# Performance work log

Measured on AMD Instinct MI355X. Metric: run time of the kernel, lower is better.

The kernel has to match this reference:

```python
import jax, jax.numpy as jnp
import numpy as np

S, B, C, HD = 3, 64, 256, 256
ZS, XS = 7, 31
EPS = 1e-5


def _bn(x, g, b, m, v):
    # inference-mode BatchNorm2d on NCHW
    inv = g / jnp.sqrt(v + EPS)
    return x * inv[None, :, None, None] + (b - m * inv)[None, :, None, None]


def _dw3(x, w):
    # depthwise 3x3 conv, VALID padding, groups = channels; w: [C,1,3,3]
    return jax.lax.conv_general_dilated(
        x, w, (1, 1), 'VALID', feature_group_count=x.shape[1],
        dimension_numbers=('NCHW', 'OIHW', 'NCHW'))


def _xcorr_depthwise(x, k):
    # Siamese depthwise cross-correlation: groups = batch*channels
    b, c, h, w = x.shape
    o = jax.lax.conv_general_dilated(
        x.reshape(1, b * c, h, w),
        k.reshape(b * c, 1, k.shape[2], k.shape[3]),
        (1, 1), 'VALID', feature_group_count=b * c,
        dimension_numbers=('NCHW', 'OIHW', 'NCHW'))
    return o.reshape(b, c, o.shape[2], o.shape[3])


def _c1(x, w):
    # 1x1 conv, no bias; w: [O,C]
    return jnp.einsum('bchw,oc->bohw', x, w)


def _forward(z_fs, x_fs, pre_w, pre_g, pre_b, pre_m, pre_v,
             head_w, head_g, head_b, head_m, head_v,
             cls_w1, cls_g, cls_b, cls_m, cls_v, cls_w2, cls_b2,
             loc_w1, loc_g, loc_b, loc_m, loc_v, loc_w2, loc_b2,
             ctr_w1, ctr_g, ctr_b, ctr_m, ctr_v, ctr_w2, ctr_b2,
             w_cls, w_loc, w_ctr):
    relu = jax.nn.relu
    cls_l, loc_l, ctr_l = [], [], []
    for i in range(S):
        search = relu(_bn(_dw3(x_fs[i], pre_w[i]), pre_g[i], pre_b[i], pre_m[i], pre_v[i]))
        kernel = relu(_bn(_dw3(z_fs[i], pre_w[i]), pre_g[i], pre_b[i], pre_m[i], pre_v[i]))
        feat = relu(_bn(_c1(_xcorr_depthwise(search, kernel), head_w[i]),
                        head_g[i], head_b[i], head_m[i], head_v[i]))

        def hd(w1, g, b, m, v, w2, b2):
            h = relu(_bn(_c1(feat, w1), g, b, m, v))
            return _c1(h, w2) + b2[None, :, None, None]

        cls_l.append(hd(cls_w1[i], cls_g[i], cls_b[i], cls_m[i], cls_v[i], cls_w2[i], cls_b2[i]))
        loc_l.append(hd(loc_w1[i], loc_g[i], loc_b[i], loc_m[i], loc_v[i], loc_w2[i], loc_b2[i]))
        ctr_l.append(hd(ctr_w1[i], ctr_g[i], ctr_b[i], ctr_m[i], ctr_v[i], ctr_w2[i], ctr_b2[i]))

    wc = jax.nn.softmax(w_cls)
    wl = jax.nn.softmax(w_loc)
    wt = jax.nn.softmax(w_ctr)
    cls = sum(cls_l[i] * wc[i] for i in range(S))
    loc = sum(loc_l[i] * wl[i] for i in range(S))
    ctr = sum(ctr_l[i] * wt[i] for i in range(S))
    return cls, loc, ctr


def setup_inputs() -> dict:
    key = jax.random.key(0)
    ks = iter(jax.random.split(key, 64))

    def rn(shape, scale=0.05):
        return jax.random.normal(next(ks), shape, jnp.float32) * scale

    def bn_params(n):
        return (jnp.ones((S, n), jnp.float32), jnp.zeros((S, n), jnp.float32),
                rn((S, n), 0.1), jax.random.uniform(next(ks), (S, n), jnp.float32) + 0.5)

    inp = {}
    inp['z_fs'] = rn((S, B, C, ZS, ZS), 1.0)
    inp['x_fs'] = rn((S, B, C, XS, XS), 1.0)
    inp['pre_w'] = rn((S, C, 1, 3, 3), 0.2)
    inp['pre_g'], inp['pre_b'], inp['pre_m'], inp['pre_v'] = bn_params(C)
    inp['head_w'] = rn((S, HD, C))
    inp['head_g'], inp['head_b'], inp['head_m'], inp['head_v'] = bn_params(HD)
    for nm, co in (('cls', 2), ('loc', 4), ('ctr', 1)):
        inp[nm + '_w1'] = rn((S, HD, HD))
        inp[nm + '_g'], inp[nm + '_b'], inp[nm + '_m'], inp[nm + '_v'] = bn_params(HD)
        inp[nm + '_w2'] = rn((S, co, HD))
        inp[nm + '_b2'] = jnp.zeros((S, co), jnp.float32)
    inp['w_cls'] = jnp.ones((S,), jnp.float32)
    inp['w_loc'] = jnp.ones((S,), jnp.float32)
    inp['w_ctr'] = jnp.ones((S,), jnp.float32)
    return inp


def reference(z_fs, x_fs, pre_w, pre_g, pre_b, pre_m, pre_v,
              head_w, head_g, head_b, head_m, head_v,
              cls_w1, cls_g, cls_b, cls_m, cls_v, cls_w2, cls_b2,
              loc_w1, loc_g, loc_b, loc_m, loc_v, loc_w2, loc_b2,
              ctr_w1, ctr_g, ctr_b, ctr_m, ctr_v, ctr_w2, ctr_b2,
              w_cls, w_loc, w_ctr):
    return _forward(z_fs, x_fs, pre_w, pre_g, pre_b, pre_m, pre_v,
                    head_w, head_g, head_b, head_m, head_v,
                    cls_w1, cls_g, cls_b, cls_m, cls_v, cls_w2, cls_b2,
                    loc_w1, loc_g, loc_b, loc_m, loc_v, loc_w2, loc_b2,
                    ctr_w1, ctr_g, ctr_b, ctr_m, ctr_v, ctr_w2, ctr_b2,
                    w_cls, w_loc, w_ctr)
```

## Files before the change

### kernel.cpp

```cpp
#include <hip/hip_runtime.h>
#include <hip/hip_bf16.h>

using bf16 = __hip_bfloat16;

#define B_  64
#define C_  256
#define HD_ 256
#define XS  31
#define XO  29
#define ZS  7
#define ZO  5
#define OSP 25
#define XO2 (XO*XO)
#define ZO2 (ZO*ZO)
#define OS2 (OSP*OSP)
#define EPSF 1e-5f

typedef __attribute__((ext_vector_type(4))) float f32x4;
typedef __attribute__((ext_vector_type(8))) short s16x8;

__device__ __forceinline__ unsigned short f2bf(float f) {
    union { float f; unsigned int u; } a; a.f = f;
    unsigned int r = a.u + 0x7FFF + ((a.u >> 16) & 1);
    return (unsigned short)(r >> 16);
}
__device__ __forceinline__ unsigned int pk2(unsigned short a, unsigned short b) {
    return (unsigned int)a | ((unsigned int)b << 16);
}

__global__ void wconv_k(const float* __restrict__ hw, const float* __restrict__ cw,
                        const float* __restrict__ lw, const float* __restrict__ tw,
                        unsigned short* __restrict__ o)
{
    int i = blockIdx.x * 256 + threadIdx.x;
    if (i >= 4 * 196608) return;
    int seg = i / 196608, r = i - seg * 196608;
    const float* s = (seg == 0) ? hw : (seg == 1) ? cw : (seg == 2) ? lw : tw;
    o[i] = f2bf(s[r]);
}

__global__ __launch_bounds__(256) void fused_pre_xcorr(
    const float* __restrict__ x, const float* __restrict__ z,
    const float* __restrict__ w, const float* __restrict__ g,
    const float* __restrict__ bb, const float* __restrict__ mm,
    const float* __restrict__ vv, unsigned short* __restrict__ out,
    int si_base)
{
    const int zs  = blockIdx.y;
    const int si  = si_base + zs;
    const int bc  = blockIdx.x;
    const int c   = bc & (C_ - 1);
    const int tid = threadIdx.x;

    __shared__ float xt[31 * 33 + 16];
    __shared__ float st[29 * 36 + 8];
    __shared__ float zt[49];
    __shared__ float ktl[25];
    __shared__ float wtl[9];

    const float* xp = x + ((size_t)si * B_ * C_ + bc) * (XS * XS);
    for (int j = tid; j < XS * XS; j += 256) xt[(j / 31) * 33 + (j % 31)] = xp[j];
    if (tid < 49) zt[tid] = z[((size_t)si * B_ * C_ + bc) * 49 + tid];
    if (tid < 9)  wtl[tid] = w[((size_t)si * C_ + c) * 9 + tid];
    const int cg = si * C_ + c;
    const float inv  = g[cg] * rsqrtf(vv[cg] + EPSF);
    const float beta = bb[cg] - mm[cg] * inv;
    __syncthreads();

    float wr[9];
    #pragma unroll
    for (int j = 0; j < 9; ++j) wr[j] = wtl[j];

    if (tid < 25) {
        int oy = tid / 5, ox = tid - (tid / 5) * 5;
        float a = 0.f;
        #pragma unroll
        for (int dy = 0; dy < 3; ++dy)
            #pragma unroll
            for (int dx = 0; dx < 3; ++dx)
                a += zt[(oy + dy) * ZS + ox + dx] * wr[dy * 3 + dx];
        ktl[tid] = fmaxf(a * inv + beta, 0.f);
    }

    if (tid < 232) {
        int r = tid >> 3, c0 = (tid & 7) * 4;
        float o0 = 0.f, o1 = 0.f, o2 = 0.f, o3 = 0.f;
        #pragma unroll
        for (int dy = 0; dy < 3; ++dy) {
            const float* row = &xt[(r + dy) * 33 + c0];
            float v0 = row[0], v1 = row[1], v2 = row[2],
                  v3 = row[3], v4 = row[4], v5 = row[5];
            float w0 = wr[dy * 3], w1 = wr[dy * 3 + 1], w2 = wr[dy * 3 + 2];
            o0 += v0 * w0 + v1 * w1 + v2 * w2;
            o1 += v1 * w0 + v2 * w1 + v3 * w2;
            o2 += v2 * w0 + v3 * w1 + v4 * w2;
            o3 += v3 * w0 + v4 * w1 + v5 * w2;
        }
        float4 res;
        res.x = fmaxf(o0 * inv + beta, 0.f);
        res.y = fmaxf(o1 * inv + beta, 0.f);
        res.z = fmaxf(o2 * inv + beta, 0.f);
        res.w = fmaxf(o3 * inv + beta, 0.f);
        *(float4*)&st[r * 36 + c0] = res;
    }
    __syncthreads();

    if (tid < 125) {
        float kt[25];
        #pragma unroll
        for (int j = 0; j < 25; ++j) kt[j] = ktl[j];
        int u = tid / 5, v0 = (tid - (tid / 5) * 5) * 5;
        float o0 = 0.f, o1 = 0.f, o2 = 0.f, o3 = 0.f, o4 = 0.f;
        #pragma unroll
        for (int p = 0; p < 5; ++p) {
            const float* row = &st[(u + p) * 36 + v0];
            float r0 = row[0], r1 = row[1], r2 = row[2], r3 = row[3], r4 = row[4],
                  r5 = row[5], r6 = row[6], r7 = row[7], r8 = row[8];
            float k0 = kt[p * 5], k1 = kt[p * 5 + 1], k2 = kt[p * 5 + 2],
                  k3 = kt[p * 5 + 3], k4 = kt[p * 5 + 4];
            o0 += r0 * k0 + r1 * k1 + r2 * k2 + r3 * k3 + r4 * k4;
            o1 += r1 * k0 + r2 * k1 + r3 * k2 + r4 * k3 + r5 * k4;
            o2 += r2 * k0 + r3 * k1 + r4 * k2 + r5 * k3 + r6 * k4;
            o3 += r3 * k0 + r4 * k1 + r5 * k2 + r6 * k3 + r7 * k4;
            o4 += r4 * k0 + r5 * k1 + r6 * k2 + r7 * k3 + r8 * k4;
        }
        unsigned short* op = out + ((size_t)zs * B_ * C_ + bc) * OS2 + u * OSP + v0;
        op[0] = f2bf(o0); op[1] = f2bf(o1); op[2] = f2bf(o2);
        op[3] = f2bf(o3); op[4] = f2bf(o4);
    }
}

__global__ __launch_bounds__(256) void c1_mfma(
    const unsigned short* __restrict__ X,
    const float* __restrict__ W,
    const unsigned short* __restrict__ Wbf,
    const float* __restrict__ g, const float* __restrict__ bb,
    const float* __restrict__ mm, const float* __restrict__ vv,
    unsigned short* __restrict__ out, int si_base)
{
    __shared__ unsigned short Abuf[4 * 128 * 8];
    __shared__ unsigned short Bbuf[4 * 128 * 8];
    __shared__ float s_inv[128], s_beta[128];

    const int tid  = threadIdx.x;
    const int wave = tid >> 6, lane = tid & 63;
    const int quad = lane >> 4, l16 = lane & 15;
    const int sb = blockIdx.x * 128;
    const int ob = blockIdx.y * 128;
    const int zs = blockIdx.z >> 6;
    const int si = si_base + zs;
    const int b  = blockIdx.z & 63;
    const int wm = (wave & 1) * 64, wn = (wave >> 1) * 64;

    const float* gs  = g  + (size_t)si * HD_;
    const float* bbs = bb + (size_t)si * HD_;
    const float* mms = mm + (size_t)si * HD_;
    const float* vvs = vv + (size_t)si * HD_;
    const float* Ws  = W  + (size_t)si * HD_ * C_;
    const unsigned short* Wbs = Wbf ? Wbf + (size_t)si * HD_ * C_ : nullptr;

    if (tid < 128) {
        int o = ob + tid;
        float iv = gs[o] * rsqrtf(vvs[o] + EPSF);
        s_inv[tid]  = iv;
        s_beta[tid] = bbs[o] - mms[o] * iv;
    }

    const int sm = tid & 127;
    const int kh = tid >> 7;
    const unsigned short* Xb = X + ((size_t)zs * B_ + b) * C_ * OS2;
    const bool npred = (sb + sm) < OS2;

    f32x4 acc[4][4];
    #pragma unroll
    for (int i = 0; i < 4; ++i)
        #pragma unroll
        for (int j = 0; j < 4; ++j)
            acc[i][j] = (f32x4){0.f, 0.f, 0.f, 0.f};

    for (int kk = 0; kk < C_; kk += 32) {
        uint4 pa0, pa1;
        if (Wbs) {
            const unsigned short* wp = Wbs + (size_t)(ob + sm) * C_ + kk + kh * 16;
            pa0 = *(const uint4*)(wp);
            pa1 = *(const uint4*)(wp + 8);
        } else {
            const float* wp = Ws + (size_t)(ob + sm) * C_ + kk + kh * 16;
            float4 w0 = *(const float4*)(wp + 0);
            float4 w1 = *(const float4*)(wp + 4);
            float4 w2 = *(const float4*)(wp + 8);
            float4 w3 = *(const float4*)(wp + 12);
            pa0.x = pk2(f2bf(w0.x), f2bf(w0.y)); pa0.y = pk2(f2bf(w0.z), f2bf(w0.w));
            pa0.z = pk2(f2bf(w1.x), f2bf(w1.y)); pa0.w = pk2(f2bf(w1.z), f2bf(w1.w));
            pa1.x = pk2(f2bf(w2.x), f2bf(w2.y)); pa1.y = pk2(f2bf(w2.z), f2bf(w2.w));
            pa1.z = pk2(f2bf(w3.x), f2bf(w3.y)); pa1.w = pk2(f2bf(w3.z), f2bf(w3.w));
        }
        *(uint4*)&Abuf[((kh * 2 + 0) * 128 + sm) * 8] = pa0;
        *(uint4*)&Abuf[((kh * 2 + 1) * 128 + sm) * 8] = pa1;

        unsigned short bu[16];
        #pragma unroll
        for (int j = 0; j < 16; ++j)
            bu[j] = npred ? Xb[(size_t)(kk + kh * 16 + j) * OS2 + sb + sm]
                          : (unsigned short)0;
        uint4 pb0, pb1;
        pb0.x = pk2(bu[0],  bu[1]);  pb0.y = pk2(bu[2],  bu[3]);
        pb0.z = pk2(bu[4],  bu[5]);  pb0.w = pk2(bu[6],  bu[7]);
        pb1.x = pk2(bu[8],  bu[9]);  pb1.y = pk2(bu[10], bu[11]);
        pb1.z = pk2(bu[12], bu[13]); pb1.w = pk2(bu[14], bu[15]);
        *(uint4*)&Bbuf[((kh * 2 + 0) * 128 + sm) * 8] = pb0;
        *(uint4*)&Bbuf[((kh * 2 + 1) * 128 + sm) * 8] = pb1;

        __syncthreads();

        s16x8 af[4], bfr[4];
        #pragma unroll
        for (int mt = 0; mt < 4; ++mt)
            af[mt] = *(const s16x8*)&Abuf[(quad * 128 + wm + mt * 16 + l16) * 8];
        #pragma unroll
        for (int nt = 0; nt < 4; ++nt)
            bfr[nt] = *(const s16x8*)&Bbuf[(quad * 128 + wn + nt * 16 + l16) * 8];
        #pragma unroll
        for (int mt = 0; mt < 4; ++mt)
            #pragma unroll
            for (int nt = 0; nt < 4; ++nt)
                acc[mt][nt] = __builtin_amdgcn_mfma_f32_16x16x32_bf16(
                    af[mt], bfr[nt], acc[mt][nt], 0, 0, 0);

        __syncthreads();
    }

    #pragma unroll
    for (int mt = 0; mt < 4; ++mt) {
        #pragma unroll
        for (int r = 0; r < 4; ++r) {
            int orow = wm + mt * 16 + quad * 4 + r;
            float iv = s_inv[orow], be = s_beta[orow];
            size_t obase = (((size_t)zs * B_ + b) * HD_ + (ob + orow)) * OS2;
            #pragma unroll
            for (int nt = 0; nt < 4; ++nt) {
                int s = sb + wn + nt * 16 + l16;
                if (s < OS2)
                    out[obase + s] = f2bf(fmaxf(acc[mt][nt][r] * iv + be, 0.f));
            }
        }
    }
}

__global__ __launch_bounds__(256) void heads3_mfma(
    const unsigned short* __restrict__ feat,
    const float* __restrict__ w1c, const float* __restrict__ w1l, const float* __restrict__ w1t,
    const unsigned short* __restrict__ Wbf,
    const float* __restrict__ gc, const float* __restrict__ bc2, const float* __restrict__ mc, const float* __restrict__ vc,
    const float* __restrict__ gl, const float* __restrict__ bl, const float* __restrict__ ml, const float* __restrict__ vl,
    const float* __restrict__ gt, const float* __restrict__ bt, const float* __restrict__ mt2, const float* __restrict__ vt,
    const float* __restrict__ w2c, const float* __restrict__ w2l, const float* __restrict__ w2t,
    const float* __restrict__ wvc, const float* __restrict__ wvl, const float* __restrict__ wvt,
    int si_base, float* __restrict__ oacc)
{
    __shared__ unsigned short Abuf[4 * 128 * 8];
    __shared__ unsigned short Bbuf[4 * 128 * 8];
    __shared__ float s_inv[128], s_beta[128];
    __shared__ float s_w2[4 * 256];

    const int tid  = threadIdx.x;
    const int wave = tid >> 6, lane = tid & 63;
    const int quad = lane >> 4, l16 = lane & 15;
    const int sb   = blockIdx.x * 128;
    const int by   = blockIdx.y;
    const int head = by >> 1;
    const int lob  = (by & 1) * 128;
    const int zs   = blockIdx.z >> 6;
    const int si   = si_base + zs;
    const int b    = blockIdx.z & 63;
    const int wm = (wave & 1) * 64, wn = (wave >> 1) * 64;

    const float* W  = (head == 0) ? w1c : (head == 1) ? w1l : w1t;
    const float* g  = (head == 0) ? gc  : (head == 1) ? gl  : gt;
    const float* bb = (head == 0) ? bc2 : (head == 1) ? bl  : bt;
    const float* mm = (head == 0) ? mc  : (head == 1) ? ml  : mt2;
    const float* vv = (head == 0) ? vc  : (head == 1) ? vl  : vt;
    const float* w2 = (head == 0) ? w2c : (head == 1) ? w2l : w2t;
    const float* wv = (head == 0) ? wvc : (head == 1) ? wvl : wvt;
    const int  CON  = (head == 0) ? 2 : (head == 1) ? 4 : 1;

    const float* Ws  = W + (size_t)si * HD_ * C_;
    const unsigned short* Wbs =
        Wbf ? Wbf + (size_t)(head + 1) * (3 * HD_ * C_) + (size_t)si * HD_ * C_ : nullptr;
    g  += (size_t)si * HD_;  bb += (size_t)si * HD_;
    mm += (size_t)si * HD_;  vv += (size_t)si * HD_;
    w2 += (size_t)si * CON * HD_;

    if (tid < 128) {
        int o = lob + tid;
        float iv = g[o] * rsqrtf(vv[o] + EPSF);
        s_inv[tid]  = iv;
        s_beta[tid] = bb[o] - mm[o] * iv;
    }
    for (int t = tid; t < CON * 256; t += 256) s_w2[t] = w2[t];

    const int sm = tid & 127;
    const int kh = tid >> 7;
    const unsigned short* Xb = feat + ((size_t)zs * B_ + b) * C_ * OS2;
    const bool npred = (sb + sm) < OS2;

    f32x4 acc[4][4];
    #pragma unroll
    for (int i = 0; i < 4; ++i)
        #pragma unroll
        for (int j = 0; j < 4; ++j)
            acc[i][j] = (f32x4){0.f, 0.f, 0.f, 0.f};

    for (int kk = 0; kk < C_; kk += 32) {
        uint4 pa0, pa1;
        if (Wbs) {
            const unsigned short* wp = Wbs + (size_t)(lob + sm) * C_ + kk + kh * 16;
            pa0 = *(const uint4*)(wp);
            pa1 = *(const uint4*)(wp + 8);
        } else {
            const float* wp = Ws + (size_t)(lob + sm) * C_ + kk + kh * 16;
            float4 w0 = *(const float4*)(wp + 0);
            float4 w1 = *(const float4*)(wp + 4);
            float4 w2v4 = *(const float4*)(wp + 8);
            float4 w3 = *(const float4*)(wp + 12);
            pa0.x = pk2(f2bf(w0.x), f2bf(w0.y)); pa0.y = pk2(f2bf(w0.z), f2bf(w0.w));
            pa0.z = pk2(f2bf(w1.x), f2bf(w1.y)); pa0.w = pk2(f2bf(w1.z), f2bf(w1.w));
            pa1.x = pk2(f2bf(w2v4.x), f2bf(w2v4.y)); pa1.y = pk2(f2bf(w2v4.z), f2bf(w2v4.w));
            pa1.z = pk2(f2bf(w3.x), f2bf(w3.y)); pa1.w = pk2(f2bf(w3.z), f2bf(w3.w));
        }
        *(uint4*)&Abuf[((kh * 2 + 0) * 128 + sm) * 8] = pa0;
        *(uint4*)&Abuf[((kh * 2 + 1) * 128 + sm) * 8] = pa1;

        unsigned short bu[16];
        #pragma unroll
        for (int j = 0; j < 16; ++j)
            bu[j] = npred ? Xb[(size_t)(kk + kh * 16 + j) * OS2 + sb + sm]
                          : (unsigned short)0;
        uint4 pb0, pb1;
        pb0.x = pk2(bu[0],  bu[1]);  pb0.y = pk2(bu[2],  bu[3]);
        pb0.z = pk2(bu[4],  bu[5]);  pb0.w = pk2(bu[6],  bu[7]);
        pb1.x = pk2(bu[8],  bu[9]);  pb1.y = pk2(bu[10], bu[11]);
        pb1.z = pk2(bu[12], bu[13]); pb1.w = pk2(bu[14], bu[15]);
        *(uint4*)&Bbuf[((kh * 2 + 0) * 128 + sm) * 8] = pb0;
        *(uint4*)&Bbuf[((kh * 2 + 1) * 128 + sm) * 8] = pb1;

        __syncthreads();

        s16x8 af[4], bfr[4];
        #pragma unroll
        for (int mt = 0; mt < 4; ++mt)
            af[mt] = *(const s16x8*)&Abuf[(quad * 128 + wm + mt * 16 + l16) * 8];
        #pragma unroll
        for (int nt = 0; nt < 4; ++nt)
            bfr[nt] = *(const s16x8*)&Bbuf[(quad * 128 + wn + nt * 16 + l16) * 8];
        #pragma unroll
        for (int mt = 0; mt < 4; ++mt)
            #pragma unroll
            for (int nt = 0; nt < 4; ++nt)
                acc[mt][nt] = __builtin_amdgcn_mfma_f32_16x16x32_bf16(
                    af[mt], bfr[nt], acc[mt][nt], 0, 0, 0);

        __syncthreads();
    }

    #pragma unroll
    for (int mt = 0; mt < 4; ++mt)
        #pragma unroll
        for (int r = 0; r < 4; ++r) {
            int orow = wm + mt * 16 + quad * 4 + r;
            float iv = s_inv[orow], be = s_beta[orow];
            #pragma unroll
            for (int nt = 0; nt < 4; ++nt)
                acc[mt][nt][r] = fmaxf(acc[mt][nt][r] * iv + be, 0.f);
        }

    const float e0 = __expf(wv[0]), e1 = __expf(wv[1]), e2 = __expf(wv[2]);
    const float wi = ((si == 0) ? e0 : (si == 1) ? e1 : e2) / (e0 + e1 + e2);

    float* obase;
    if (head == 0)      obase = oacc + (size_t)b * 2 * OS2;
    else if (head == 1) obase = oacc + (size_t)B_ * 2 * OS2 + (size_t)b * 4 * OS2;
    else                obase = oacc + (size_t)B_ * 6 * OS2 + (size_t)b * OS2;

    for (int co = 0; co < CON; ++co) {
        float red[4] = {0.f, 0.f, 0.f, 0.f};
        #pragma unroll
        for (int mt = 0; mt < 4; ++mt)
            #pragma unroll
            for (int r = 0; r < 4; ++r) {
                float w2v = s_w2[co * 256 + lob + wm + mt * 16 + quad * 4 + r];
                #pragma unroll
                for (int nt = 0; nt < 4; ++nt)
                    red[nt] += w2v * acc[mt][nt][r];
            }
        #pragma unroll
        for (int nt = 0; nt < 4; ++nt) {
            red[nt] += __shfl_xor(red[nt], 16);
            red[nt] += __shfl_xor(red[nt], 32);
        }
        if (quad == 0) {
            #pragma unroll
            for (int nt = 0; nt < 4; ++nt) {
                int s = sb + wn + nt * 16 + l16;
                if (s < OS2)
                    atomicAdd(obase + (size_t)co * OS2 + s, wi * red[nt]);
            }
        }
    }
}

__global__ void bias_out(float* __restrict__ out,
    const float* __restrict__ cb2, const float* __restrict__ lb2,
    const float* __restrict__ tb2, const float* __restrict__ wvc,
    const float* __restrict__ wvl, const float* __restrict__ wvt)
{
    int n = blockIdx.x * 256 + threadIdx.x;
    if (n >= B_ * 7 * OS2) return;
    float bias;
    if (n < B_ * 2 * OS2) {
        float e0 = __expf(wvc[0]), e1 = __expf(wvc[1]), e2 = __expf(wvc[2]);
        int co = (n / OS2) & 1;
        bias = (e0 * cb2[co] + e1 * cb2[2 + co] + e2 * cb2[4 + co]) / (e0 + e1 + e2);
    } else if (n < B_ * 6 * OS2) {
        float e0 = __expf(wvl[0]), e1 = __expf(wvl[1]), e2 = __expf(wvl[2]);
        int co = ((n - B_ * 2 * OS2) / OS2) & 3;
        bias = (e0 * lb2[co] + e1 * lb2[4 + co] + e2 * lb2[8 + co]) / (e0 + e1 + e2);
    } else {
        float e0 = __expf(wvt[0]), e1 = __expf(wvt[1]), e2 = __expf(wvt[2]);
        bias = (e0 * tb2[0] + e1 * tb2[1] + e2 * tb2[2]) / (e0 + e1 + e2);
    }
    out[n] += bias;
}

__global__ void fillf_k(float* __restrict__ out, int n, float v)
{
    int i = blockIdx.x * 256 + threadIdx.x;
    if (i < n) out[i] = v;
}

extern "C" void kernel_launch(void* const* d_in, const int* in_sizes, int n_in,
                              void* d_out, int out_size, void* d_ws, size_t ws_size,
                              hipStream_t stream)
{
    static const int EXP_SIZES[36] = {
        2408448, 47235072, 6912,
        768, 768, 768, 768,
        196608, 768, 768, 768, 768,
        196608, 768, 768, 768, 768, 1536, 6,
        196608, 768, 768, 768, 768, 3072, 12,
        196608, 768, 768, 768, 768, 768, 3,
        3, 3, 3
    };
    int bad = -1;
    if (n_in != 36) bad = 99;
    else {
        for (int i = 0; i < 36; ++i)
            if (in_sizes[i] != EXP_SIZES[i]) { bad = i; break; }
    }
    if (bad < 0 && ws_size < (size_t)40960000) bad = 90;
    if (bad < 0 && out_size != 280000) bad = 95;
    if (bad >= 0) {
        fillf_k<<<(out_size + 255) / 256, 256, 0, stream>>>(
            (float*)d_out, out_size, 500.f + 4.f * bad);
        return;
    }

    const float* z_fs   = (const float*)d_in[0];
    const float* x_fs   = (const float*)d_in[1];
    const float* pre_w  = (const float*)d_in[2];
    const float* pre_g  = (const float*)d_in[3];
    const float* pre_b  = (const float*)d_in[4];
    const float* pre_m  = (const float*)d_in[5];
    const float* pre_v  = (const float*)d_in[6];
    const float* head_w = (const float*)d_in[7];
    const float* head_g = (const float*)d_in[8];
    const float* head_b = (const float*)d_in[9];
    const float* head_m = (const float*)d_in[10];
    const float* head_v = (const float*)d_in[11];
    const float* cls_w1 = (const float*)d_in[12];
    const float* cls_g  = (const float*)d_in[13];
    const float* cls_b  = (const float*)d_in[14];
    const float* cls_m  = (const float*)d_in[15];
    const float* cls_v  = (const float*)d_in[16];
    const float* cls_w2 = (const float*)d_in[17];
    const float* cls_b2 = (const float*)d_in[18];
    const float* loc_w1 = (const float*)d_in[19];
    const float* loc_g  = (const float*)d_in[20];
    const float* loc_b  = (const float*)d_in[21];
    const float* loc_m  = (const float*)d_in[22];
    const float* loc_v  = (const float*)d_in[23];
    const float* loc_w2 = (const float*)d_in[24];
    const float* loc_b2 = (const float*)d_in[25];
    const float* ctr_w1 = (const float*)d_in[26];
    const float* ctr_g  = (const float*)d_in[27];
    const float* ctr_b  = (const float*)d_in[28];
    const float* ctr_m  = (const float*)d_in[29];
    const float* ctr_v  = (const float*)d_in[30];
    const float* ctr_w2 = (const float*)d_in[31];
    const float* ctr_b2 = (const float*)d_in[32];
    const float* w_cls  = (const float*)d_in[33];
    const float* w_loc  = (const float*)d_in[34];
    const float* w_ctr  = (const float*)d_in[35];

    const int OUT_N = B_ * 7 * OS2;
    const size_t stageEl = (size_t)B_ * C_ * OS2;
    const size_t WBF_EL = (size_t)4 * 3 * HD_ * C_;
    const bool batched = ws_size >= (6 * stageEl + WBF_EL) * sizeof(unsigned short);

    hipMemsetAsync(d_out, 0, (size_t)OUT_N * sizeof(float), stream);

    if (batched) {
        unsigned short* xc   = (unsigned short*)d_ws;
        unsigned short* feat = xc + 3 * stageEl;
        unsigned short* wbf  = feat + 3 * stageEl;

        wconv_k<<<(4 * 196608 + 255) / 256, 256, 0, stream>>>(
            head_w, cls_w1, loc_w1, ctr_w1, wbf);

        fused_pre_xcorr<<<dim3(B_ * C_, 3), 256, 0, stream>>>(
            x_fs, z_fs, pre_w, pre_g, pre_b, pre_m, pre_v, xc, 0);

        c1_mfma<<<dim3(5, 2, 3 * B_), 256, 0, stream>>>(
            xc, head_w, wbf, head_g, head_b, head_m, head_v, feat, 0);

        heads3_mfma<<<dim3(5, 6, 3 * B_), 256, 0, stream>>>(
            feat, cls_w1, loc_w1, ctr_w1, wbf,
            cls_g, cls_b, cls_m, cls_v,
            loc_g, loc_b, loc_m, loc_v,
            ctr_g, ctr_b, ctr_m, ctr_v,
            cls_w2, loc_w2, ctr_w2,
            w_cls, w_loc, w_ctr, 0, (float*)d_out);
    } else {
        unsigned short* xc   = (unsigned short*)d_ws;
        unsigned short* feat = xc + stageEl;

        for (int i = 0; i < 3; ++i) {
            fused_pre_xcorr<<<dim3(B_ * C_, 1), 256, 0, stream>>>(
                x_fs, z_fs, pre_w, pre_g, pre_b, pre_m, pre_v, xc, i);

            c1_mfma<<<dim3(5, 2, B_), 256, 0, stream>>>(
                xc, head_w, nullptr, head_g, head_b, head_m, head_v, feat, i);

            heads3_mfma<<<dim3(5, 6, B_), 256, 0, stream>>>(
                feat, cls_w1, loc_w1, ctr_w1, nullptr,
                cls_g, cls_b, cls_m, cls_v,
                loc_g, loc_b, loc_m, loc_v,
                ctr_g, ctr_b, ctr_m, ctr_v,
                cls_w2, loc_w2, ctr_w2,
                w_cls, w_loc, w_ctr, i, (float*)d_out);
        }
    }

    bias_out<<<(OUT_N + 255) / 256, 256, 0, stream>>>(
        (float*)d_out, cls_b2, loc_b2, ctr_b2, w_cls, w_loc, w_ctr);
}
```

Baseline: 594.1 us.

## Process two channels per block in fused depthwise pre-conv and xcorr kernel

Each block of the fused pre-conv/xcorr kernel now handles two adjacent (batch,channel) planes instead of one, halving the grid. Threads that were idle in the xcorr phase (only 125 of 256 active) now cover both channels. The 3x3 depthwise conv gives each thread two output rows, reusing shared input rows. The goal is better thread utilisation and fewer blocks, at the cost of more shared memory and registers per block.

```diff
diff --git a/kernel.cpp b/kernel.cpp
--- a/kernel.cpp
+++ b/kernel.cpp
@@ -16,6 +16,10 @@
 #define OS2 (OSP*OSP)
 #define EPSF 1e-5f
 
+#define XCST 976
+#define SRS  36
+#define SCST (29 * SRS)
+
 typedef __attribute__((ext_vector_type(4))) float f32x4;
 typedef __attribute__((ext_vector_type(8))) short s16x8;
 
@@ -48,85 +52,137 @@
 {
     const int zs  = blockIdx.y;
     const int si  = si_base + zs;
-    const int bc  = blockIdx.x;
-    const int c   = bc & (C_ - 1);
+    const int bc0 = blockIdx.x * 2;
     const int tid = threadIdx.x;
 
-    __shared__ float xt[31 * 33 + 16];
-    __shared__ float st[29 * 36 + 8];
-    __shared__ float zt[49];
-    __shared__ float ktl[25];
-    __shared__ float wtl[9];
-
-    const float* xp = x + ((size_t)si * B_ * C_ + bc) * (XS * XS);
-    for (int j = tid; j < XS * XS; j += 256) xt[(j / 31) * 33 + (j % 31)] = xp[j];
-    if (tid < 49) zt[tid] = z[((size_t)si * B_ * C_ + bc) * 49 + tid];
-    if (tid < 9)  wtl[tid] = w[((size_t)si * C_ + c) * 9 + tid];
-    const int cg = si * C_ + c;
-    const float inv  = g[cg] * rsqrtf(vv[cg] + EPSF);
-    const float beta = bb[cg] - mm[cg] * inv;
+    __shared__ float xt[2 * XCST + 8];
+    __shared__ float st[2 * SCST + 16];
+    __shared__ float zt[2 * 49];
+    __shared__ float ktl[2 * 25];
+    __shared__ float wtl[2 * 9];
+    __shared__ float sprm[4];
+
+    const float* xp = x + ((size_t)si * B_ * C_ + bc0) * (XS * XS);
+    #pragma unroll
+    for (int k2 = 0; k2 < 8; ++k2) {
+        int idx = tid + k2 * 256;
+        if (idx < 2 * XS * XS) {
+            int off = idx + (idx >= XS * XS ? (XCST - XS * XS) : 0);
+            xt[off] = xp[idx];
+        }
+    }
+    if (tid < 98) zt[tid] = z[((size_t)si * B_ * C_ + bc0) * 49 + tid];
+    if (tid < 18) wtl[tid] = w[((size_t)si * C_ + (bc0 & (C_ - 1))) * 9 + tid];
+    if (tid < 2) {
+        int cg = si * C_ + (bc0 & (C_ - 1)) + tid;
+        float iv = g[cg] * rsqrtf(vv[cg] + EPSF);
+        sprm[tid * 2]     = iv;
+        sprm[tid * 2 + 1] = bb[cg] - mm[cg] * iv;
+    }
     __syncthreads();
 
-    float wr[9];
-    #pragma unroll
-    for (int j = 0; j < 9; ++j) wr[j] = wtl[j];
-
-    if (tid < 25) {
-        int oy = tid / 5, ox = tid - (tid / 5) * 5;
+    if (tid < 50) {
+        int ch = (tid >= 25) ? 1 : 0;
+        int l  = tid - ch * 25;
+        int oy = l / 5, ox = l - (l / 5) * 5;
+        const float* zb = &zt[ch * 49];
+        const float* wb = &wtl[ch * 9];
         float a = 0.f;
         #pragma unroll
         for (int dy = 0; dy < 3; ++dy)
             #pragma unroll
             for (int dx = 0; dx < 3; ++dx)
-                a += zt[(oy + dy) * ZS + ox + dx] * wr[dy * 3 + dx];
-        ktl[tid] = fmaxf(a * inv + beta, 0.f);
-    }
-
-    if (tid < 232) {
-        int r = tid >> 3, c0 = (tid & 7) * 4;
-        float o0 = 0.f, o1 = 0.f, o2 = 0.f, o3 = 0.f;
-        #pragma unroll
-        for (int dy = 0; dy < 3; ++dy) {
-            const float* row = &xt[(r + dy) * 33 + c0];
-            float v0 = row[0], v1 = row[1], v2 = row[2],
-                  v3 = row[3], v4 = row[4], v5 = row[5];
-            float w0 = wr[dy * 3], w1 = wr[dy * 3 + 1], w2 = wr[dy * 3 + 2];
-            o0 += v0 * w0 + v1 * w1 + v2 * w2;
-            o1 += v1 * w0 + v2 * w1 + v3 * w2;
-            o2 += v2 * w0 + v3 * w1 + v4 * w2;
-            o3 += v3 * w0 + v4 * w1 + v5 * w2;
-        }
-        float4 res;
-        res.x = fmaxf(o0 * inv + beta, 0.f);
-        res.y = fmaxf(o1 * inv + beta, 0.f);
-        res.z = fmaxf(o2 * inv + beta, 0.f);
-        res.w = fmaxf(o3 * inv + beta, 0.f);
-        *(float4*)&st[r * 36 + c0] = res;
+                a += zb[(oy + dy) * ZS + ox + dx] * wb[dy * 3 + dx];
+        ktl[ch * 25 + l] = fmaxf(a * sprm[ch * 2] + sprm[ch * 2 + 1], 0.f);
+    }
+
+    if (tid < 240) {
+        int ch    = (tid >= 120) ? 1 : 0;
+        int rem   = tid - ch * 120;
+        int strip = rem >> 3;
+        int cgp   = rem & 7;
+        int r0    = strip * 2;
+        const float* base = &xt[ch * XCST + r0 * XS + cgp * 4];
+        const float* wb   = &wtl[ch * 9];
+        float w0 = wb[0], w1 = wb[1], w2 = wb[2],
+              w3 = wb[3], w4 = wb[4], w5 = wb[5],
+              w6 = wb[6], w7 = wb[7], w8 = wb[8];
+        const float inv  = sprm[ch * 2];
+        const float beta = sprm[ch * 2 + 1];
+
+        float a0 = 0.f, a1 = 0.f, a2 = 0.f, a3 = 0.f;
+        float b0 = 0.f, b1 = 0.f, b2 = 0.f, b3 = 0.f;
+        #pragma unroll
+        for (int dy = 0; dy < 4; ++dy) {
+            const float* rp = base + dy * XS;
+            float v0 = rp[0], v1 = rp[1], v2 = rp[2],
+                  v3 = rp[3], v4 = rp[4], v5 = rp[5];
+            if (dy < 3) {
+                float u0 = (dy == 0) ? w0 : (dy == 1) ? w3 : w6;
+                float u1 = (dy == 0) ? w1 : (dy == 1) ? w4 : w7;
+                float u2 = (dy == 0) ? w2 : (dy == 1) ? w5 : w8;
+                a0 += v0 * u0 + v1 * u1 + v2 * u2;
+                a1 += v1 * u0 + v2 * u1 + v3 * u2;
+                a2 += v2 * u0 + v3 * u1 + v4 * u2;
+                a3 += v3 * u0 + v4 * u1 + v5 * u2;
+            }
+            if (dy >= 1) {
+                float u0 = (dy == 1) ? w0 : (dy == 2) ? w3 : w6;
+                float u1 = (dy == 1) ? w1 : (dy == 2) ? w4 : w7;
+                float u2 = (dy == 1) ? w2 : (dy == 2) ? w5 : w8;
+                b0 += v0 * u0 + v1 * u1 + v2 * u2;
+                b1 += v1 * u0 + v2 * u1 + v3 * u2;
+                b2 += v2 * u0 + v3 * u1 + v4 * u2;
+                b3 += v3 * u0 + v4 * u1 + v5 * u2;
+            }
+        }
+        float4 ra;
+        ra.x = fmaxf(a0 * inv + beta, 0.f);
+        ra.y = fmaxf(a1 * inv + beta, 0.f);
+        ra.z = fmaxf(a2 * inv + beta, 0.f);
+        ra.w = fmaxf(a3 * inv + beta, 0.f);
+        *(float4*)&st[ch * SCST + r0 * SRS + cgp * 4] = ra;
+        if (r0 + 1 < XO) {
+            float4 rb;
+            rb.x = fmaxf(b0 * inv + beta, 0.f);
+            rb.y = fmaxf(b1 * inv + beta, 0.f);
+            rb.z = fmaxf(b2 * inv + beta, 0.f);
+            rb.w = fmaxf(b3 * inv + beta, 0.f);
+            *(float4*)&st[ch * SCST + (r0 + 1) * SRS + cgp * 4] = rb;
+        }
     }
     __syncthreads();
 
-    if (tid < 125) {
-        float kt[25];
-        #pragma unroll
-        for (int j = 0; j < 25; ++j) kt[j] = ktl[j];
-        int u = tid / 5, v0 = (tid - (tid / 5) * 5) * 5;
-        float o0 = 0.f, o1 = 0.f, o2 = 0.f, o3 = 0.f, o4 = 0.f;
-        #pragma unroll
-        for (int p = 0; p < 5; ++p) {
-            const float* row = &st[(u + p) * 36 + v0];
-            float r0 = row[0], r1 = row[1], r2 = row[2], r3 = row[3], r4 = row[4],
-                  r5 = row[5], r6 = row[6], r7 = row[7], r8 = row[8];
-            float k0 = kt[p * 5], k1 = kt[p * 5 + 1], k2 = kt[p * 5 + 2],
-                  k3 = kt[p * 5 + 3], k4 = kt[p * 5 + 4];
-            o0 += r0 * k0 + r1 * k1 + r2 * k2 + r3 * k3 + r4 * k4;
-            o1 += r1 * k0 + r2 * k1 + r3 * k2 + r4 * k3 + r5 * k4;
-            o2 += r2 * k0 + r3 * k1 + r4 * k2 + r5 * k3 + r6 * k4;
-            o3 += r3 * k0 + r4 * k1 + r5 * k2 + r6 * k3 + r7 * k4;
-            o4 += r4 * k0 + r5 * k1 + r6 * k2 + r7 * k3 + r8 * k4;
-        }
-        unsigned short* op = out + ((size_t)zs * B_ * C_ + bc) * OS2 + u * OSP + v0;
-        op[0] = f2bf(o0); op[1] = f2bf(o1); op[2] = f2bf(o2);
-        op[3] = f2bf(o3); op[4] = f2bf(o4);
+    {
+        const int ch = tid >> 7;
+        const int l  = tid & 127;
+        if (l < 125) {
+            const float* kb = &ktl[ch * 25];
+            float kt[25];
+            #pragma unroll
+            for (int j = 0; j < 25; ++j) kt[j] = kb[j];
+            int u  = l / 5;
+            int v0 = (l - u * 5) * 5;
+            const float* sbase = &st[ch * SCST + u * SRS + v0];
+            float o0 = 0.f, o1 = 0.f, o2 = 0.f, o3 = 0.f, o4 = 0.f;
+            #pragma unroll
+            for (int p = 0; p < 5; ++p) {
+                const float* rp = sbase + p * SRS;
+                float r0 = rp[0], r1 = rp[1], r2 = rp[2], r3 = rp[3], r4 = rp[4],
+                      r5 = rp[5], r6 = rp[6], r7 = rp[7], r8 = rp[8];
+                float k0 = kt[p * 5], k1 = kt[p * 5 + 1], k2 = kt[p * 5 + 2],
+                      k3 = kt[p * 5 + 3], k4 = kt[p * 5 + 4];
+                o0 += r0 * k0 + r1 * k1 + r2 * k2 + r3 * k3 + r4 * k4;
+                o1 += r1 * k0 + r2 * k1 + r3 * k2 + r4 * k3 + r5 * k4;
+                o2 += r2 * k0 + r3 * k1 + r4 * k2 + r5 * k3 + r6 * k4;
+                o3 += r3 * k0 + r4 * k1 + r5 * k2 + r6 * k3 + r7 * k4;
+                o4 += r4 * k0 + r5 * k1 + r6 * k2 + r7 * k3 + r8 * k4;
+            }
+            unsigned short* op = out + ((size_t)zs * B_ * C_ + bc0 + ch) * OS2
+                                     + u * OSP + v0;
+            op[0] = f2bf(o0); op[1] = f2bf(o1); op[2] = f2bf(o2);
+            op[3] = f2bf(o3); op[4] = f2bf(o4);
+        }
     }
 }
 
@@ -517,7 +573,7 @@
         wconv_k<<<(4 * 196608 + 255) / 256, 256, 0, stream>>>(
             head_w, cls_w1, loc_w1, ctr_w1, wbf);
 
-        fused_pre_xcorr<<<dim3(B_ * C_, 3), 256, 0, stream>>>(
+        fused_pre_xcorr<<<dim3(B_ * C_ / 2, 3), 256, 0, stream>>>(
             x_fs, z_fs, pre_w, pre_g, pre_b, pre_m, pre_v, xc, 0);
 
         c1_mfma<<<dim3(5, 2, 3 * B_), 256, 0, stream>>>(
@@ -535,7 +591,7 @@
         unsigned short* feat = xc + stageEl;
 
         for (int i = 0; i < 3; ++i) {
-            fused_pre_xcorr<<<dim3(B_ * C_, 1), 256, 0, stream>>>(
+            fused_pre_xcorr<<<dim3(B_ * C_ / 2, 1), 256, 0, stream>>>(
                 x_fs, z_fs, pre_w, pre_g, pre_b, pre_m, pre_v, xc, i);
 
             c1_mfma<<<dim3(5, 2, B_), 256, 0, stream>>>(
```

Measured after the change: 564.0 us. -5.1%, faster.
